# Performance work log

Hardware: AMD Instinct MI355X
Metric: run time of the kernel (lower is better)

The kernel has to match this reference:

```python
import jax, jax.numpy as jnp
import numpy as np

B, T, C = 2, 2048, 2048
H, HKV, DH = 32, 8, 64
G = H // HKV  # kv_group_size = 4


def setup_inputs() -> dict:
    key = jax.random.key(0)
    k1, k2, k3, k4 = jax.random.split(key, 4)
    x = jax.random.normal(k1, (B, T, C), dtype=jnp.float32)
    Wq = jax.random.normal(k2, (C, C), dtype=jnp.float32) * 0.02
    Wkv = jax.random.normal(k3, (2 * HKV * DH, C), dtype=jnp.float32) * 0.02
    Wo = jax.random.normal(k4, (C, C), dtype=jnp.float32) * 0.02
    # RoPE tables: cos/sin of shape (T, DH/2)
    inv_freq = 1.0 / (10000.0 ** (jnp.arange(0, DH // 2, dtype=jnp.float32) / (DH // 2)))
    ang = jnp.arange(T, dtype=jnp.float32)[:, None] * inv_freq[None, :]  # (T, DH/2)
    return {"x": x, "cos": jnp.cos(ang), "sin": jnp.sin(ang), "Wq": Wq, "Wkv": Wkv, "Wo": Wo}


def _rotate_half(t):
    t1, t2 = jnp.split(t, 2, axis=-1)
    return jnp.concatenate([-t2, t1], axis=-1)


def reference(x, cos, sin, Wq, Wkv, Wo):
    # Projections (torch Linear: y = x @ W.T)
    q = (x @ Wq.T).reshape(B, T, H, DH).transpose(0, 2, 1, 3)      # (B,H,T,DH)
    kv = (x @ Wkv.T).reshape(B, T, 2, HKV, DH)
    k = kv[:, :, 0].transpose(0, 2, 1, 3)                          # (B,HKV,T,DH)
    v = kv[:, :, 1].transpose(0, 2, 1, 3)
    # RoPE
    cos2 = jnp.concatenate([cos, cos], axis=-1)[None, None]        # (1,1,T,DH)
    sin2 = jnp.concatenate([sin, sin], axis=-1)[None, None]
    q = q * cos2 + _rotate_half(q) * sin2
    k = k * cos2 + _rotate_half(k) * sin2
    # Grouped-query attention without materializing repeated K/V:
    # view q as (B, HKV, G, T, DH) and contract against shared K/V heads.
    qg = q.reshape(B, HKV, G, T, DH)
    scale = 1.0 / jnp.sqrt(jnp.float32(DH))
    scores = jnp.einsum("bhgqd,bhkd->bhgqk", qg, k) * scale        # (B,HKV,G,T,T)
    causal = jnp.tril(jnp.ones((T, T), dtype=bool))
    scores = jnp.where(causal[None, None, None], scores, -jnp.inf)
    attn = jax.nn.softmax(scores, axis=-1)
    out = jnp.einsum("bhgqk,bhkd->bhgqd", attn, v)                 # (B,HKV,G,T,DH)
    out = out.reshape(B, H, T, DH).transpose(0, 2, 1, 3).reshape(B, T, C)
    return out @ Wo.T
```

## Files before the change

### kernel.cpp

```cpp
#include <hip/hip_runtime.h>
#include <hip/hip_bf16.h>

#define B_    2
#define T_    2048
#define C_    2048
#define H_    32
#define HKV_  8
#define DH_   64
#define NQKV  3072
#define KOFF  2048
#define VOFF  2560

typedef __attribute__((ext_vector_type(4))) float f32x4;
typedef __attribute__((ext_vector_type(16))) float f32x16;
typedef __attribute__((ext_vector_type(8))) short bf16x8;
typedef __attribute__((ext_vector_type(4))) short s16x4;

__device__ __forceinline__ float bf2f(short s) {
  union { unsigned u; float f; } v; v.u = ((unsigned)(unsigned short)s) << 16; return v.f;
}
__device__ __forceinline__ short f2bf(float f) {
  union { float f; unsigned u; } v; v.f = f;
  unsigned u = v.u + 0x7fffu + ((v.u >> 16) & 1u);
  return (short)(u >> 16);
}
__device__ __forceinline__ unsigned pk2(float lo, float hi) {
  union { __hip_bfloat162 b; unsigned u; } c;
  c.b = __float22bfloat162_rn(make_float2(lo, hi));
  return c.u;
}

__device__ __forceinline__ void gload_lds16(const void* g, void* l) {
  __builtin_amdgcn_global_load_lds((const __attribute__((address_space(1))) void*)g,
                                   (__attribute__((address_space(3))) void*)l, 16, 0, 0);
}

__global__ void cvt4_kernel(const float* __restrict__ x, const float* __restrict__ Wq,
                            const float* __restrict__ Wkv, const float* __restrict__ Wo,
                            short* __restrict__ dst) {
  const int g = blockIdx.x * 256 + threadIdx.x;
  const float* src; int off;
  if (g < 2097152)      { src = x;   off = g; }
  else if (g < 3145728) { src = Wq;  off = g - 2097152; }
  else if (g < 3670016) { src = Wkv; off = g - 3145728; }
  else                  { src = Wo;  off = g - 3670016; }
  const float4 v = reinterpret_cast<const float4*>(src)[off];
  s16x4 o; o[0] = f2bf(v.x); o[1] = f2bf(v.y); o[2] = f2bf(v.z); o[3] = f2bf(v.w);
  reinterpret_cast<s16x4*>(dst)[g] = o;
}

__global__ void rope_kernel(short* __restrict__ qkv, const float* __restrict__ cosT,
                            const float* __restrict__ sinT) {
  const int r = blockIdx.y;
  const int p = blockIdx.x * 256 + threadIdx.x;
  const int t = r & (T_ - 1);
  const int dd = p & 31;
  int col0; float sc;
  if (p < 1024) { int hh = p >> 5; col0 = hh * 64 + dd; sc = 0.18033688011112042f; }
  else          { int hh = (p - 1024) >> 5; col0 = KOFF + hh * 64 + dd; sc = 1.0f; }
  const float c = cosT[t * 32 + dd], s = sinT[t * 32 + dd];
  short* base = qkv + (size_t)r * NQKV;
  const float x1 = bf2f(base[col0]);
  const float x2 = bf2f(base[col0 + 32]);
  base[col0]      = f2bf((x1 * c - x2 * s) * sc);
  base[col0 + 32] = f2bf((x2 * c + x1 * s) * sc);
}

__global__ void vtrans_kernel(const short* __restrict__ qkv, short* __restrict__ vT) {
  __shared__ short tile[64][72];
  const int tid = threadIdx.x;
  const int tt = blockIdx.x, bh = blockIdx.y;
  const int b = bh >> 3, hk = bh & 7;
#pragma unroll
  for (int i = 0; i < 2; ++i) {
    int c = tid + i * 256;
    int r = c >> 3, s = c & 7;
    bf16x8 v = *reinterpret_cast<const bf16x8*>(
        qkv + ((size_t)(b * T_ + tt * 64 + r)) * NQKV + VOFF + hk * 64 + s * 8);
#pragma unroll
    for (int e = 0; e < 8; ++e) tile[s * 8 + e][r] = v[e];
  }
  __syncthreads();
#pragma unroll
  for (int i = 0; i < 2; ++i) {
    int c = tid + i * 256;
    int d = c >> 3, s = c & 7;
    bf16x8 o;
#pragma unroll
    for (int e = 0; e < 8; ++e) o[e] = tile[d][s * 8 + e];
    *reinterpret_cast<bf16x8*>(vT + ((size_t)bh * 64 + d) * T_ + tt * 64 + s * 8) = o;
  }
}

template <int OUT_BF16>
__global__ __launch_bounds__(256) void gemm_bt(const short* __restrict__ A,
                                               const short* __restrict__ Bm,
                                               void* __restrict__ Cm,
                                               int M, int N, int K) {
  __shared__ __attribute__((aligned(16))) short Alds[128 * 32];
  __shared__ __attribute__((aligned(16))) short Blds[128 * 32];
  const int tid = threadIdx.x;
  const int w = tid >> 6, lane = tid & 63, g = lane >> 4, l15 = lane & 15;
  const int wm = (w >> 1) * 64, wn = (w & 1) * 64;

  int bid = blockIdx.y * gridDim.x + blockIdx.x;
  const int nwg = gridDim.x * gridDim.y;
  int wg = (nwg & 7) ? bid : ((bid & 7) * (nwg >> 3) + (bid >> 3));
  const int m0 = (wg / gridDim.x) * 128, n0 = (wg % gridDim.x) * 128;

  f32x4 acc[4][4] = {};

  for (int k0 = 0; k0 < K; k0 += 32) {
#pragma unroll
    for (int i = 0; i < 2; ++i) {
      int c = w * 128 + i * 64 + lane;
      int row = c >> 2, slot = c & 3;
      int ks = slot ^ ((row >> 1) & 3);
      gload_lds16(A + (size_t)(m0 + row) * K + k0 + ks * 8,
                  Alds + (w * 128 + i * 64) * 8);
      gload_lds16(Bm + (size_t)(n0 + row) * K + k0 + ks * 8,
                  Blds + (w * 128 + i * 64) * 8);
    }
    __syncthreads();
    bf16x8 af[4], bf[4];
#pragma unroll
    for (int mi = 0; mi < 4; ++mi) {
      int ra = wm + mi * 16 + l15;
      af[mi] = *reinterpret_cast<const bf16x8*>(Alds + ra * 32 + (g ^ ((ra >> 1) & 3)) * 8);
      int rb = wn + mi * 16 + l15;
      bf[mi] = *reinterpret_cast<const bf16x8*>(Blds + rb * 32 + (g ^ ((rb >> 1) & 3)) * 8);
    }
#pragma unroll
    for (int mi = 0; mi < 4; ++mi)
#pragma unroll
      for (int ni = 0; ni < 4; ++ni)
        acc[mi][ni] = __builtin_amdgcn_mfma_f32_16x16x32_bf16(af[mi], bf[ni], acc[mi][ni], 0, 0, 0);
    __syncthreads();
  }

#pragma unroll
  for (int mi = 0; mi < 4; ++mi)
#pragma unroll
    for (int ni = 0; ni < 4; ++ni) {
      const int m = m0 + wm + mi * 16 + g * 4;
      const int n = n0 + wn + ni * 16 + l15;
      if (OUT_BF16) {
        short* Cp = (short*)Cm;
#pragma unroll
        for (int r = 0; r < 4; ++r) Cp[(size_t)(m + r) * N + n] = f2bf(acc[mi][ni][r]);
      } else {
        float* Cp = (float*)Cm;
#pragma unroll
        for (int r = 0; r < 4; ++r) Cp[(size_t)(m + r) * N + n] = acc[mi][ni][r];
      }
    }
}

__global__ __launch_bounds__(256) void attn_kernel(const short* __restrict__ qkv,
                                                   const short* __restrict__ vT,
                                                   short* __restrict__ out) {
  __shared__ __attribute__((aligned(16))) short Klds[2][64 * 64];
  __shared__ __attribute__((aligned(16))) short Vlds[2][64 * 64];

  const int tid = threadIdx.x, w = tid >> 6, lane = tid & 63;
  const int l31 = lane & 31, hl = lane >> 5;

  const int bid = blockIdx.x;
  const int xcd = bid & 7, k = bid >> 3;
  const int qh = xcd * 8 + (k & 7);
  const int qi = k >> 3;
  const int m_ = qi & 3, d_ = qi >> 2;
  const int qt = (d_ & 1) ? (2 * m_ + (d_ >> 1)) : (15 - (d_ >> 1) - 2 * m_);
  const int b = qh >> 5, h = qh & 31, hk = h >> 2;

  const int nt = 2 * qt + 2;
  const int myend = 2 * qt + (w >> 1) + 1;
  const size_t browbase = (size_t)b * T_;
  const size_t qrow = browbase + qt * 128 + w * 32 + l31;

  bf16x8 qf[4];
#pragma unroll
  for (int s = 0; s < 4; ++s)
    qf[s] = *reinterpret_cast<const bf16x8*>(qkv + qrow * NQKV + h * 64 + s * 16 + hl * 8);

  const short* kg = qkv + browbase * NQKV + KOFF + hk * 64;
  const short* vg = vT + ((size_t)(b * HKV_ + hk)) * 64 * T_;

  float m_run = -1e30f, l_run = 0.f;
  f32x16 o0 = {}, o1 = {};

  auto STAGE = [&](int kt, int buf) {
    const int kv0 = kt * 64;
#pragma unroll
    for (int i = 0; i < 2; ++i) {
      const int c = w * 128 + i * 64 + lane;
      const int j = c >> 3, slot = c & 7;
      gload_lds16(kg + (size_t)(kv0 + j) * NQKV + (slot ^ (j & 7)) * 8,
                  &Klds[buf][(w * 128 + i * 64) * 8]);
      gload_lds16(vg + (size_t)j * T_ + kv0 + (slot ^ (j & 7)) * 8,
                  &Vlds[buf][(w * 128 + i * 64) * 8]);
    }
  };

#define KFRAG(TAU, S) (*reinterpret_cast<const bf16x8*>( \
    Kc + ((TAU) * 32 + l31) * 64 + (((hl + 2 * (S)) ^ (l31 & 7)) * 8)))
#define VFRAG(DT, S) (*reinterpret_cast<const bf16x8*>( \
    Vc + ((DT) * 32 + l31) * 64 + (((hl + 2 * (S)) ^ (l31 & 7)) * 8)))

  STAGE(0, 0);
  __syncthreads();

  for (int t = 0; t < nt; ++t) {
    const int cur = t & 1;
    if (t + 1 < nt) STAGE(t + 1, cur ^ 1);
    const short* Kc = &Klds[cur][0];
    const short* Vc = &Vlds[cur][0];

    if (t < myend) {
      f32x16 st0 = {}, st1 = {};
#pragma unroll
      for (int s = 0; s < 4; ++s) {
        st0 = __builtin_amdgcn_mfma_f32_32x32x16_bf16(KFRAG(0, s), qf[s], st0, 0, 0, 0);
        st1 = __builtin_amdgcn_mfma_f32_32x32x16_bf16(KFRAG(1, s), qf[s], st1, 0, 0, 0);
      }

      if (t == myend - 1) {
        const int dq = ((w & 1) << 5) + l31;
#pragma unroll
        for (int r = 0; r < 16; ++r) {
          const int j0 = (r & 3) + 8 * (r >> 2) + 4 * hl;
          if (j0 > dq)      st0[r] = -1e30f;
          if (j0 + 32 > dq) st1[r] = -1e30f;
        }
      }

      float tmax = -1e30f;
#pragma unroll
      for (int r = 0; r < 16; ++r) tmax = fmaxf(tmax, fmaxf(st0[r], st1[r]));
      tmax = fmaxf(tmax, __shfl_xor(tmax, 32));
      if (__any(tmax > m_run + 8.0f)) {
        const float m_new = fmaxf(m_run, tmax);
        const float corr = exp2f(m_run - m_new);
        l_run *= corr;
#pragma unroll
        for (int r = 0; r < 16; ++r) { o0[r] *= corr; o1[r] *= corr; }
        m_run = m_new;
      }
      float tsum = 0.f;
#pragma unroll
      for (int r = 0; r < 16; ++r) {
        st0[r] = exp2f(st0[r] - m_run); tsum += st0[r];
        st1[r] = exp2f(st1[r] - m_run); tsum += st1[r];
      }
      tsum += __shfl_xor(tsum, 32);
      l_run += tsum;

      unsigned u0[8], u1[8];
#pragma unroll
      for (int kk = 0; kk < 8; ++kk) {
        u0[kk] = pk2(st0[2 * kk], st0[2 * kk + 1]);
        u1[kk] = pk2(st1[2 * kk], st1[2 * kk + 1]);
      }

#define PV_STEP(S, UU)                                                        \
      {                                                                       \
        const int base_ = ((S) & 1) * 4;                                      \
        unsigned x0 = UU[base_ + 0], y0 = UU[base_ + 2];                      \
        unsigned x1 = UU[base_ + 1], y1 = UU[base_ + 3];                      \
        asm volatile("v_permlane32_swap_b32 %0, %1" : "+v"(x0), "+v"(y0));    \
        asm volatile("v_permlane32_swap_b32 %0, %1" : "+v"(x1), "+v"(y1));    \
        union { unsigned uw[4]; bf16x8 v8; } fr_;                             \
        fr_.uw[0] = x0; fr_.uw[1] = x1; fr_.uw[2] = y0; fr_.uw[3] = y1;       \
        o0 = __builtin_amdgcn_mfma_f32_32x32x16_bf16(VFRAG(0, S), fr_.v8, o0, 0, 0, 0); \
        o1 = __builtin_amdgcn_mfma_f32_32x32x16_bf16(VFRAG(1, S), fr_.v8, o1, 0, 0, 0); \
      }
      PV_STEP(0, u0)
      PV_STEP(1, u0)
      PV_STEP(2, u1)
      PV_STEP(3, u1)
#undef PV_STEP
    }
    __syncthreads();
  }

  const float inv = 1.0f / l_run;
  short* obase = out + qrow * C_ + h * 64;
#pragma unroll
  for (int rr = 0; rr < 4; ++rr) {
    s16x4 ov;
#pragma unroll
    for (int e = 0; e < 4; ++e) ov[e] = f2bf(o0[rr * 4 + e] * inv);
    *reinterpret_cast<s16x4*>(obase + rr * 8 + hl * 4) = ov;
  }
#pragma unroll
  for (int rr = 0; rr < 4; ++rr) {
    s16x4 ov;
#pragma unroll
    for (int e = 0; e < 4; ++e) ov[e] = f2bf(o1[rr * 4 + e] * inv);
    *reinterpret_cast<s16x4*>(obase + 32 + rr * 8 + hl * 4) = ov;
  }
#undef KFRAG
#undef VFRAG
}

extern "C" void kernel_launch(void* const* d_in, const int* in_sizes, int n_in,
                              void* d_out, int out_size, void* d_ws, size_t ws_size,
                              hipStream_t stream) {
  const float* x    = (const float*)d_in[0];
  const float* cosT = (const float*)d_in[1];
  const float* sinT = (const float*)d_in[2];
  const float* Wq   = (const float*)d_in[3];
  const float* Wkv  = (const float*)d_in[4];
  const float* Wo   = (const float*)d_in[5];

  short* xb   = (short*)d_ws;
  short* wqkv = xb + (size_t)4096 * 2048;
  short* wob  = wqkv + (size_t)3072 * 2048;
  short* qkv  = wob + (size_t)2048 * 2048;
  short* aout = qkv + (size_t)4096 * 3072;
  short* vTb  = xb;

  cvt4_kernel<<<18432, 256, 0, stream>>>(x, Wq, Wkv, Wo, (short*)d_ws);

  gemm_bt<1><<<dim3(24, 32), 256, 0, stream>>>(xb, wqkv, qkv, 4096, 3072, 2048);
  rope_kernel<<<dim3(5, 4096), 256, 0, stream>>>(qkv, cosT, sinT);
  vtrans_kernel<<<dim3(32, 16), 256, 0, stream>>>(qkv, vTb);
  attn_kernel<<<1024, 256, 0, stream>>>(qkv, vTb, aout);
  gemm_bt<0><<<dim3(16, 32), 256, 0, stream>>>(aout, wob, (float*)d_out, 4096, 2048, 2048);
}
```

Before: 341.2 us.

## Fuse RoPE into QKV GEMM epilogue and pair causal query tiles per block

Removes the standalone RoPE kernel by applying the rotation and the softmax scale in the QKV GEMM epilogue while the fp32 accumulators are still in registers. This avoids a separate read-modify-write pass over Q and K in bf16. The attention kernel now handles two query tiles per block, p and 15-p, so every block does the same amount of causal work, and the grid is halved to 512 blocks. It also adds s_setprio around the MFMA sections; in exchange each block carries more register state and runs a longer loop.

Measured after the change: 331.7 us. 2.8% less time.

```diff
diff --git a/kernel.cpp b/kernel.cpp
--- a/kernel.cpp
+++ b/kernel.cpp
@@ -49,23 +49,6 @@
   reinterpret_cast<s16x4*>(dst)[g] = o;
 }
 
-__global__ void rope_kernel(short* __restrict__ qkv, const float* __restrict__ cosT,
-                            const float* __restrict__ sinT) {
-  const int r = blockIdx.y;
-  const int p = blockIdx.x * 256 + threadIdx.x;
-  const int t = r & (T_ - 1);
-  const int dd = p & 31;
-  int col0; float sc;
-  if (p < 1024) { int hh = p >> 5; col0 = hh * 64 + dd; sc = 0.18033688011112042f; }
-  else          { int hh = (p - 1024) >> 5; col0 = KOFF + hh * 64 + dd; sc = 1.0f; }
-  const float c = cosT[t * 32 + dd], s = sinT[t * 32 + dd];
-  short* base = qkv + (size_t)r * NQKV;
-  const float x1 = bf2f(base[col0]);
-  const float x2 = bf2f(base[col0 + 32]);
-  base[col0]      = f2bf((x1 * c - x2 * s) * sc);
-  base[col0 + 32] = f2bf((x2 * c + x1 * s) * sc);
-}
-
 __global__ void vtrans_kernel(const short* __restrict__ qkv, short* __restrict__ vT) {
   __shared__ short tile[64][72];
   const int tid = threadIdx.x;
@@ -92,10 +75,12 @@
   }
 }
 
-template <int OUT_BF16>
+template <int MODE>
 __global__ __launch_bounds__(256) void gemm_bt(const short* __restrict__ A,
                                                const short* __restrict__ Bm,
                                                void* __restrict__ Cm,
+                                               const float* __restrict__ cosT,
+                                               const float* __restrict__ sinT,
                                                int M, int N, int K) {
   __shared__ __attribute__((aligned(16))) short Alds[128 * 32];
   __shared__ __attribute__((aligned(16))) short Blds[128 * 32];
@@ -138,13 +123,32 @@
     __syncthreads();
   }
 
+  if (MODE == 2 && n0 < VOFF) {
+    const float sc = (n0 < KOFF) ? 0.18033688011112042f : 1.0f;
+#pragma unroll
+    for (int mi = 0; mi < 4; ++mi)
+#pragma unroll
+      for (int ni = 0; ni < 2; ++ni) {
+        const int dd = ni * 16 + l15;
+#pragma unroll
+        for (int r = 0; r < 4; ++r) {
+          const int t = (m0 + wm + mi * 16 + g * 4 + r) & (T_ - 1);
+          const float c = cosT[t * 32 + dd] * sc;
+          const float s = sinT[t * 32 + dd] * sc;
+          const float a = acc[mi][ni][r], b2 = acc[mi][ni + 2][r];
+          acc[mi][ni][r]     = a * c - b2 * s;
+          acc[mi][ni + 2][r] = b2 * c + a * s;
+        }
+      }
+  }
+
 #pragma unroll
   for (int mi = 0; mi < 4; ++mi)
 #pragma unroll
     for (int ni = 0; ni < 4; ++ni) {
       const int m = m0 + wm + mi * 16 + g * 4;
       const int n = n0 + wn + ni * 16 + l15;
-      if (OUT_BF16) {
+      if (MODE) {
         short* Cp = (short*)Cm;
 #pragma unroll
         for (int r = 0; r < 4; ++r) Cp[(size_t)(m + r) * N + n] = f2bf(acc[mi][ni][r]);
@@ -166,38 +170,42 @@
   const int l31 = lane & 31, hl = lane >> 5;
 
   const int bid = blockIdx.x;
-  const int xcd = bid & 7, k = bid >> 3;
-  const int qh = xcd * 8 + (k & 7);
-  const int qi = k >> 3;
-  const int m_ = qi & 3, d_ = qi >> 2;
-  const int qt = (d_ & 1) ? (2 * m_ + (d_ >> 1)) : (15 - (d_ >> 1) - 2 * m_);
+  const int xcd = bid & 7, slot = bid >> 3;
+  const int qh = xcd * 8 + (slot & 7);
+  const int p = slot >> 3;
+  const int qtB = 15 - p;
   const int b = qh >> 5, h = qh & 31, hk = h >> 2;
 
-  const int nt = 2 * qt + 2;
-  const int myend = 2 * qt + (w >> 1) + 1;
+  const int nTA = 2 * p + 2;
+  const int myendA = 2 * p + (w >> 1) + 1;
+  const int myendB = 2 * qtB + (w >> 1) + 1;
   const size_t browbase = (size_t)b * T_;
-  const size_t qrow = browbase + qt * 128 + w * 32 + l31;
-
-  bf16x8 qf[4];
-#pragma unroll
-  for (int s = 0; s < 4; ++s)
-    qf[s] = *reinterpret_cast<const bf16x8*>(qkv + qrow * NQKV + h * 64 + s * 16 + hl * 8);
+  const size_t qrowA = browbase + p * 128 + w * 32 + l31;
+  const size_t qrowB = browbase + qtB * 128 + w * 32 + l31;
+
+  bf16x8 qfA[4], qfB[4];
+#pragma unroll
+  for (int s = 0; s < 4; ++s) {
+    qfA[s] = *reinterpret_cast<const bf16x8*>(qkv + qrowA * NQKV + h * 64 + s * 16 + hl * 8);
+    qfB[s] = *reinterpret_cast<const bf16x8*>(qkv + qrowB * NQKV + h * 64 + s * 16 + hl * 8);
+  }
 
   const short* kg = qkv + browbase * NQKV + KOFF + hk * 64;
   const short* vg = vT + ((size_t)(b * HKV_ + hk)) * 64 * T_;
 
   float m_run = -1e30f, l_run = 0.f;
   f32x16 o0 = {}, o1 = {};
+  const short *Kc, *Vc;
 
   auto STAGE = [&](int kt, int buf) {
     const int kv0 = kt * 64;
 #pragma unroll
     for (int i = 0; i < 2; ++i) {
       const int c = w * 128 + i * 64 + lane;
-      const int j = c >> 3, slot = c & 7;
-      gload_lds16(kg + (size_t)(kv0 + j) * NQKV + (slot ^ (j & 7)) * 8,
+      const int j = c >> 3, sl = c & 7;
+      gload_lds16(kg + (size_t)(kv0 + j) * NQKV + (sl ^ (j & 7)) * 8,
                   &Klds[buf][(w * 128 + i * 64) * 8]);
-      gload_lds16(vg + (size_t)j * T_ + kv0 + (slot ^ (j & 7)) * 8,
+      gload_lds16(vg + (size_t)j * T_ + kv0 + (sl ^ (j & 7)) * 8,
                   &Vlds[buf][(w * 128 + i * 64) * 8]);
     }
   };
@@ -207,98 +215,122 @@
 #define VFRAG(DT, S) (*reinterpret_cast<const bf16x8*>( \
     Vc + ((DT) * 32 + l31) * 64 + (((hl + 2 * (S)) ^ (l31 & 7)) * 8)))
 
+  auto TILE_STEP = [&](const bf16x8* qf, bool diag) {
+    f32x16 st0 = {}, st1 = {};
+    __builtin_amdgcn_s_setprio(1);
+#pragma unroll
+    for (int s = 0; s < 4; ++s) {
+      st0 = __builtin_amdgcn_mfma_f32_32x32x16_bf16(KFRAG(0, s), qf[s], st0, 0, 0, 0);
+      st1 = __builtin_amdgcn_mfma_f32_32x32x16_bf16(KFRAG(1, s), qf[s], st1, 0, 0, 0);
+    }
+    __builtin_amdgcn_s_setprio(0);
+
+    if (diag) {
+      const int dq = ((w & 1) << 5) + l31;
+#pragma unroll
+      for (int r = 0; r < 16; ++r) {
+        const int j0 = (r & 3) + 8 * (r >> 2) + 4 * hl;
+        if (j0 > dq)      st0[r] = -1e30f;
+        if (j0 + 32 > dq) st1[r] = -1e30f;
+      }
+    }
+
+    float tmax = -1e30f;
+#pragma unroll
+    for (int r = 0; r < 16; ++r) tmax = fmaxf(tmax, fmaxf(st0[r], st1[r]));
+    tmax = fmaxf(tmax, __shfl_xor(tmax, 32));
+    if (__any(tmax > m_run + 8.0f)) {
+      const float m_new = fmaxf(m_run, tmax);
+      const float corr = exp2f(m_run - m_new);
+      l_run *= corr;
+#pragma unroll
+      for (int r = 0; r < 16; ++r) { o0[r] *= corr; o1[r] *= corr; }
+      m_run = m_new;
+    }
+    float tsum = 0.f;
+#pragma unroll
+    for (int r = 0; r < 16; ++r) {
+      st0[r] = exp2f(st0[r] - m_run); tsum += st0[r];
+      st1[r] = exp2f(st1[r] - m_run); tsum += st1[r];
+    }
+    tsum += __shfl_xor(tsum, 32);
+    l_run += tsum;
+
+    unsigned u0[8], u1[8];
+#pragma unroll
+    for (int kk = 0; kk < 8; ++kk) {
+      u0[kk] = pk2(st0[2 * kk], st0[2 * kk + 1]);
+      u1[kk] = pk2(st1[2 * kk], st1[2 * kk + 1]);
+    }
+
+    __builtin_amdgcn_s_setprio(1);
+#define PV_STEP(S, UU)                                                        \
+    {                                                                         \
+      const int base_ = ((S) & 1) * 4;                                        \
+      unsigned x0 = UU[base_ + 0], y0 = UU[base_ + 2];                        \
+      unsigned x1 = UU[base_ + 1], y1 = UU[base_ + 3];                        \
+      asm volatile("v_permlane32_swap_b32 %0, %1" : "+v"(x0), "+v"(y0));      \
+      asm volatile("v_permlane32_swap_b32 %0, %1" : "+v"(x1), "+v"(y1));      \
+      union { unsigned uw[4]; bf16x8 v8; } fr_;                               \
+      fr_.uw[0] = x0; fr_.uw[1] = x1; fr_.uw[2] = y0; fr_.uw[3] = y1;         \
+      o0 = __builtin_amdgcn_mfma_f32_32x32x16_bf16(VFRAG(0, S), fr_.v8, o0, 0, 0, 0); \
+      o1 = __builtin_amdgcn_mfma_f32_32x32x16_bf16(VFRAG(1, S), fr_.v8, o1, 0, 0, 0); \
+    }
+    PV_STEP(0, u0)
+    PV_STEP(1, u0)
+    PV_STEP(2, u1)
+    PV_STEP(3, u1)
+#undef PV_STEP
+    __builtin_amdgcn_s_setprio(0);
+  };
+
+  auto EPI = [&](size_t qrow) {
+    const float inv = 1.0f / l_run;
+    short* obase = out + qrow * C_ + h * 64;
+#pragma unroll
+    for (int rr = 0; rr < 4; ++rr) {
+      s16x4 ov;
+#pragma unroll
+      for (int e = 0; e < 4; ++e) ov[e] = f2bf(o0[rr * 4 + e] * inv);
+      *reinterpret_cast<s16x4*>(obase + rr * 8 + hl * 4) = ov;
+    }
+#pragma unroll
+    for (int rr = 0; rr < 4; ++rr) {
+      s16x4 ov;
+#pragma unroll
+      for (int e = 0; e < 4; ++e) ov[e] = f2bf(o1[rr * 4 + e] * inv);
+      *reinterpret_cast<s16x4*>(obase + 32 + rr * 8 + hl * 4) = ov;
+    }
+  };
+
   STAGE(0, 0);
   __syncthreads();
 
-  for (int t = 0; t < nt; ++t) {
+  for (int t = 0; t < 34; ++t) {
     const int cur = t & 1;
-    if (t + 1 < nt) STAGE(t + 1, cur ^ 1);
-    const short* Kc = &Klds[cur][0];
-    const short* Vc = &Vlds[cur][0];
-
-    if (t < myend) {
-      f32x16 st0 = {}, st1 = {};
-#pragma unroll
-      for (int s = 0; s < 4; ++s) {
-        st0 = __builtin_amdgcn_mfma_f32_32x32x16_bf16(KFRAG(0, s), qf[s], st0, 0, 0, 0);
-        st1 = __builtin_amdgcn_mfma_f32_32x32x16_bf16(KFRAG(1, s), qf[s], st1, 0, 0, 0);
+    if (t + 1 < 34) {
+      const int kn = (t + 1 < nTA) ? (t + 1) : (t + 1 - nTA);
+      STAGE(kn, cur ^ 1);
+    }
+    Kc = &Klds[cur][0];
+    Vc = &Vlds[cur][0];
+
+    if (t < myendA) {
+      TILE_STEP(qfA, t == myendA - 1);
+    } else {
+      if (t == myendA) {
+        EPI(qrowA);
+        m_run = -1e30f; l_run = 0.f;
+#pragma unroll
+        for (int r = 0; r < 16; ++r) { o0[r] = 0.f; o1[r] = 0.f; }
       }
-
-      if (t == myend - 1) {
-        const int dq = ((w & 1) << 5) + l31;
-#pragma unroll
-        for (int r = 0; r < 16; ++r) {
-          const int j0 = (r & 3) + 8 * (r >> 2) + 4 * hl;
-          if (j0 > dq)      st0[r] = -1e30f;
-          if (j0 + 32 > dq) st1[r] = -1e30f;
-        }
-      }
-
-      float tmax = -1e30f;
-#pragma unroll
-      for (int r = 0; r < 16; ++r) tmax = fmaxf(tmax, fmaxf(st0[r], st1[r]));
-      tmax = fmaxf(tmax, __shfl_xor(tmax, 32));
-      if (__any(tmax > m_run + 8.0f)) {
-        const float m_new = fmaxf(m_run, tmax);
-        const float corr = exp2f(m_run - m_new);
-        l_run *= corr;
-#pragma unroll
-        for (int r = 0; r < 16; ++r) { o0[r] *= corr; o1[r] *= corr; }
-        m_run = m_new;
-      }
-      float tsum = 0.f;
-#pragma unroll
-      for (int r = 0; r < 16; ++r) {
-        st0[r] = exp2f(st0[r] - m_run); tsum += st0[r];
-        st1[r] = exp2f(st1[r] - m_run); tsum += st1[r];
-      }
-      tsum += __shfl_xor(tsum, 32);
-      l_run += tsum;
-
-      unsigned u0[8], u1[8];
-#pragma unroll
-      for (int kk = 0; kk < 8; ++kk) {
-        u0[kk] = pk2(st0[2 * kk], st0[2 * kk + 1]);
-        u1[kk] = pk2(st1[2 * kk], st1[2 * kk + 1]);
-      }
-
-#define PV_STEP(S, UU)                                                        \
-      {                                                                       \
-        const int base_ = ((S) & 1) * 4;                                      \
-        unsigned x0 = UU[base_ + 0], y0 = UU[base_ + 2];                      \
-        unsigned x1 = UU[base_ + 1], y1 = UU[base_ + 3];                      \
-        asm volatile("v_permlane32_swap_b32 %0, %1" : "+v"(x0), "+v"(y0));    \
-        asm volatile("v_permlane32_swap_b32 %0, %1" : "+v"(x1), "+v"(y1));    \
-        union { unsigned uw[4]; bf16x8 v8; } fr_;                             \
-        fr_.uw[0] = x0; fr_.uw[1] = x1; fr_.uw[2] = y0; fr_.uw[3] = y1;       \
-        o0 = __builtin_amdgcn_mfma_f32_32x32x16_bf16(VFRAG(0, S), fr_.v8, o0, 0, 0, 0); \
-        o1 = __builtin_amdgcn_mfma_f32_32x32x16_bf16(VFRAG(1, S), fr_.v8, o1, 0, 0, 0); \
-      }
-      PV_STEP(0, u0)
-      PV_STEP(1, u0)
-      PV_STEP(2, u1)
-      PV_STEP(3, u1)
-#undef PV_STEP
+      const int tb = t - nTA;
+      if (tb >= 0 && tb < myendB) TILE_STEP(qfB, tb == myendB - 1);
     }
     __syncthreads();
   }
 
-  const float inv = 1.0f / l_run;
-  short* obase = out + qrow * C_ + h * 64;
-#pragma unroll
-  for (int rr = 0; rr < 4; ++rr) {
-    s16x4 ov;
-#pragma unroll
-    for (int e = 0; e < 4; ++e) ov[e] = f2bf(o0[rr * 4 + e] * inv);
-    *reinterpret_cast<s16x4*>(obase + rr * 8 + hl * 4) = ov;
-  }
-#pragma unroll
-  for (int rr = 0; rr < 4; ++rr) {
-    s16x4 ov;
-#pragma unroll
-    for (int e = 0; e < 4; ++e) ov[e] = f2bf(o1[rr * 4 + e] * inv);
-    *reinterpret_cast<s16x4*>(obase + 32 + rr * 8 + hl * 4) = ov;
-  }
+  EPI(qrowB);
 #undef KFRAG
 #undef VFRAG
 }
@@ -322,9 +354,8 @@
 
   cvt4_kernel<<<18432, 256, 0, stream>>>(x, Wq, Wkv, Wo, (short*)d_ws);
 
-  gemm_bt<1><<<dim3(24, 32), 256, 0, stream>>>(xb, wqkv, qkv, 4096, 3072, 2048);
-  rope_kernel<<<dim3(5, 4096), 256, 0, stream>>>(qkv, cosT, sinT);
+  gemm_bt<2><<<dim3(24, 32), 256, 0, stream>>>(xb, wqkv, qkv, cosT, sinT, 4096, 3072, 2048);
   vtrans_kernel<<<dim3(32, 16), 256, 0, stream>>>(qkv, vTb);
-  attn_kernel<<<1024, 256, 0, stream>>>(qkv, vTb, aout);
-  gemm_bt<0><<<dim3(16, 32), 256, 0, stream>>>(aout, wob, (float*)d_out, 4096, 2048, 2048);
-}
+  attn_kernel<<<512, 256, 0, stream>>>(qkv, vTb, aout);
+  gemm_bt<0><<<dim3(16, 32), 256, 0, stream>>>(aout, wob, (float*)d_out, cosT, sinT, 4096, 2048, 2048);
+}
```
